# Performance work log

Hardware: AMD Instinct MI355X
Metric: run time of the kernel (lower is better)

Reference implementation:

```python
import jax, jax.numpy as jnp
import numpy as np

N, E = 50000, 800000
DN, DE, H, C = 64, 64, 4, 2
DH = DN // H


def setup_inputs() -> dict:
    key = jax.random.key(0)
    ks = jax.random.split(key, 12)
    def lin(k, fan_in, fan_out):
        return jax.random.normal(k, (fan_in, fan_out), dtype=jnp.float32) / np.sqrt(fan_in)
    return {
        "node_features": jax.random.normal(ks[0], (N, DN), dtype=jnp.float32),
        "edge_features": jax.random.normal(ks[1], (E, DE), dtype=jnp.float32),
        "edge_index": jax.random.randint(ks[2], (2, E), 0, N, dtype=jnp.int64),
        "Wq": lin(ks[3], DN, DN),
        "Wk": lin(ks[4], DN, DN),
        "Wv": lin(ks[5], DN, DN),
        "We": lin(ks[6], DE, DN),
        "Wo": lin(ks[7], DN, DN),
        "W1": lin(ks[8], 2 * DN + DE, DE),
        "b1": jnp.zeros((DE,), dtype=jnp.float32),
        "W2": lin(ks[9], DE, C),
        "b2": jnp.zeros((C,), dtype=jnp.float32),
    }


def reference(node_features, edge_features, edge_index, Wq, Wk, Wv, We, Wo, W1, b1, W2, b2):
    n = node_features.shape[0]
    src, tgt = edge_index[0], edge_index[1]

    # --- NodeAttention: multi-head attention over incoming edges ---
    q = (node_features @ Wq).reshape(n, H, DH)
    k = (node_features @ Wk).reshape(n, H, DH)
    v = (node_features @ Wv).reshape(n, H, DH)
    ep = (edge_features @ We).reshape(-1, H, DH)          # [E,H,DH]

    scores = jnp.sum(q[tgt] * (k[src] + ep), axis=-1) / np.sqrt(DH)  # [E,H]
    smax = jax.ops.segment_max(scores, tgt, num_segments=n)          # [N,H]
    ex = jnp.exp(scores - smax[tgt])
    denom = jax.ops.segment_sum(ex, tgt, num_segments=n)
    alpha = ex / (denom[tgt] + 1e-9)                                 # [E,H]

    msg = (alpha[..., None] * (v[src] + ep)).reshape(-1, H * DH)     # [E,DN]
    agg = jax.ops.segment_sum(msg, tgt, num_segments=n)              # [N,DN]
    new_nodes = node_features + agg @ Wo                             # residual

    # --- edge classifier: gather endpoints, concat edge feats, MLP+GELU ---
    edge_repr = jnp.concatenate([new_nodes[src], new_nodes[tgt], edge_features], axis=-1)
    h = jax.nn.gelu(edge_repr @ W1 + b1, approximate=False)
    return h @ W2 + b2
```

## Files before the change

kernel.cpp:

```cpp
#include <hip/hip_runtime.h>
#include <math.h>

typedef __attribute__((ext_vector_type(8))) short bf16x8;
typedef __attribute__((ext_vector_type(4))) float f32x4;

__device__ __forceinline__ short f2bf(float f) {
    unsigned u = __float_as_uint(f);
    unsigned r = (u + 0x7FFFu + ((u >> 16) & 1u)) >> 16;
    return (short)r;
}

__device__ __forceinline__ int swz(int row, int kbyte) {
    return kbyte ^ ((row & 7) << 4);
}

__global__ __launch_bounds__(256) void qkv_kernel(
    const float* __restrict__ x,
    const float* __restrict__ Wq, const float* __restrict__ Wk, const float* __restrict__ Wv,
    float* __restrict__ q, float* __restrict__ k, float* __restrict__ v, int N)
{
    __shared__ float sW[3][64][64];
    __shared__ float sx[4][64];
    int t = threadIdx.x;
    for (int i = t; i < 4096; i += 256) {
        sW[0][i >> 6][i & 63] = Wq[i];
        sW[1][i >> 6][i & 63] = Wk[i];
        sW[2][i >> 6][i & 63] = Wv[i];
    }
    __syncthreads();
    int c = t & 63, sub = t >> 6;
    for (int base = blockIdx.x * 4; base < N; base += gridDim.x * 4) {
        int n = base + sub;
        if (n < N) sx[sub][c] = x[(size_t)n * 64 + c];
        __syncthreads();
        if (n < N) {
            float aq = 0.f, ak = 0.f, av = 0.f;
            #pragma unroll
            for (int i = 0; i < 64; i++) {
                float xv = sx[sub][i];
                aq += xv * sW[0][i][c];
                ak += xv * sW[1][i][c];
                av += xv * sW[2][i][c];
            }
            q[(size_t)n * 64 + c] = aq;
            k[(size_t)n * 64 + c] = ak;
            v[(size_t)n * 64 + c] = av;
        }
        __syncthreads();
    }
}

__device__ __forceinline__ void stage_w64T(const float* __restrict__ W, short* sWT, int t) {
    for (int i = t; i < 4096; i += 256) {
        int k = i >> 6, n = i & 63;
        short vv = f2bf(W[i]);
        int kb = k * 2;
        int off = n * 128 + (swz(n, kb & ~15) | (kb & 15));
        *(short*)((char*)sWT + off) = vv;
    }
}

__device__ __forceinline__ void ep_mfma(
    const float* __restrict__ ef, const short* sWeT, float* ep_lds,
    size_t tile64, int t)
{
    int lane = t & 63, w = t >> 6;
    f32x4 acc[4];
    #pragma unroll
    for (int nt = 0; nt < 4; nt++) acc[nt] = (f32x4){0.f, 0.f, 0.f, 0.f};

    #pragma unroll
    for (int kk = 0; kk < 2; kk++) {
        const float* base = ef + (tile64 + (size_t)(w * 16 + (lane & 15))) * 64
                               + kk * 32 + (lane >> 4) * 8;
        float4 x0 = *(const float4*)(base);
        float4 x1 = *(const float4*)(base + 4);
        bf16x8 a;
        a[0] = f2bf(x0.x); a[1] = f2bf(x0.y); a[2] = f2bf(x0.z); a[3] = f2bf(x0.w);
        a[4] = f2bf(x1.x); a[5] = f2bf(x1.y); a[6] = f2bf(x1.z); a[7] = f2bf(x1.w);
        #pragma unroll
        for (int nt = 0; nt < 4; nt++) {
            int n = nt * 16 + (lane & 15);
            int kb = kk * 64 + (lane >> 4) * 16;
            bf16x8 b = *(const bf16x8*)((const char*)sWeT + n * 128 + swz(n, kb));
            acc[nt] = __builtin_amdgcn_mfma_f32_16x16x32_bf16(a, b, acc[nt], 0, 0, 0);
        }
    }
    #pragma unroll
    for (int nt = 0; nt < 4; nt++)
        #pragma unroll
        for (int r = 0; r < 4; r++) {
            int row = w * 16 + (lane >> 4) * 4 + r;
            int col = nt * 16 + (lane & 15);
            ep_lds[row * 66 + col] = acc[nt][r];
        }
}

__global__ __launch_bounds__(256) void edge_kernel(
    const float* __restrict__ ef, const int* __restrict__ eidx,
    const float* __restrict__ q, const float* __restrict__ k,
    const float* __restrict__ v, const float* __restrict__ We,
    float* __restrict__ denom, float* __restrict__ agg, int E)
{
    __shared__ short sWeT[4096];
    __shared__ float ep_lds[64 * 66];
    __shared__ float ex_lds[64 * 4];
    __shared__ int sidx[64], tidx[64];
    int t = threadIdx.x;
    stage_w64T(We, sWeT, t);
    __syncthreads();

    int lane = t & 63, w = t >> 6;
    int ntiles = E >> 6;
    for (int tile = blockIdx.x; tile < ntiles; tile += gridDim.x) {
        size_t tile64 = (size_t)tile * 64;
        if (t < 64) {
            sidx[t] = eidx[tile64 + t];
            tidx[t] = eidx[(size_t)E + tile64 + t];
        }
        __syncthreads();
        ep_mfma(ef, sWeT, ep_lds, tile64, t);
        __syncthreads();

        {
            int e_loc = t >> 2, h = t & 3;
            int src = sidx[e_loc], tgt = tidx[e_loc];
            const float4* qp = (const float4*)(q + (size_t)tgt * 64 + h * 16);
            const float4* kp = (const float4*)(k + (size_t)src * 64 + h * 16);
            const float* epp = ep_lds + e_loc * 66 + h * 16;
            float s = 0.f;
            #pragma unroll
            for (int j = 0; j < 4; j++) {
                float4 qq = qp[j];
                float4 kk = kp[j];
                s += qq.x * (kk.x + epp[j * 4 + 0]);
                s += qq.y * (kk.y + epp[j * 4 + 1]);
                s += qq.z * (kk.z + epp[j * 4 + 2]);
                s += qq.w * (kk.w + epp[j * 4 + 3]);
            }
            float ex = __expf(s * 0.25f);
            ex_lds[e_loc * 4 + h] = ex;
            atomicAdd(&denom[(size_t)tgt * 4 + h], ex);
        }
        __syncthreads();

        #pragma unroll 4
        for (int i = 0; i < 16; i++) {
            int e_loc = w * 16 + i;
            int src = sidx[e_loc], tgt = tidx[e_loc];
            float ex = ex_lds[e_loc * 4 + (lane >> 4)];
            float msg = ex * (v[(size_t)src * 64 + lane] + ep_lds[e_loc * 66 + lane]);
            atomicAdd(&agg[(size_t)tgt * 64 + lane], msg);
        }
        __syncthreads();
    }
}

__global__ __launch_bounds__(256) void wo_kernel(
    const float* __restrict__ agg, const float* __restrict__ denom,
    const float* __restrict__ x,
    const float* __restrict__ Wo, float* __restrict__ out, int N)
{
    __shared__ float sW[64][64];
    __shared__ float sx[4][64];
    int t = threadIdx.x;
    for (int i = t; i < 4096; i += 256) sW[i >> 6][i & 63] = Wo[i];
    __syncthreads();
    int c = t & 63, sub = t >> 6;
    for (int base = blockIdx.x * 4; base < N; base += gridDim.x * 4) {
        int n = base + sub;
        if (n < N) {
            float d = denom[(size_t)n * 4 + (c >> 4)] + 1e-9f;
            sx[sub][c] = agg[(size_t)n * 64 + c] / d;
        }
        __syncthreads();
        if (n < N) {
            float acc = 0.f;
            #pragma unroll
            for (int i = 0; i < 64; i++) acc += sx[sub][i] * sW[i][c];
            out[(size_t)n * 64 + c] = x[(size_t)n * 64 + c] + acc;
        }
        __syncthreads();
    }
}

__global__ __launch_bounds__(256, 4) void cls_kernel(
    const float* __restrict__ nn, const float* __restrict__ ef,
    const int* __restrict__ eidx,
    const float* __restrict__ W1, const float* __restrict__ b1,
    const float* __restrict__ W2, const float* __restrict__ b2,
    float* __restrict__ out, int E)
{
    __shared__ short sWt1[64 * 192];
    __shared__ float sW2[128];
    __shared__ float sb1[64];
    __shared__ float sb2[2];
    __shared__ int sidx[64], tidx[64];
    int t = threadIdx.x;
    for (int i = t; i < 192 * 64; i += 256) {
        int k = i >> 6, n = i & 63;
        short vv = f2bf(W1[i]);
        int kb = k * 2;
        int off = n * 384 + (swz(n, kb & ~15) | (kb & 15));
        *(short*)((char*)sWt1 + off) = vv;
    }
    if (t < 128) sW2[t] = W2[t];
    if (t < 64) sb1[t] = b1[t];
    if (t < 2) sb2[t] = b2[t];
    __syncthreads();

    int lane = t & 63, w = t >> 6;
    int ntiles = E >> 6;
    for (int tile = blockIdx.x; tile < ntiles; tile += gridDim.x) {
        size_t tile64 = (size_t)tile * 64;
        if (t < 64) {
            sidx[t] = eidx[tile64 + t];
            tidx[t] = eidx[(size_t)E + tile64 + t];
        }
        __syncthreads();

        f32x4 acc[4];
        #pragma unroll
        for (int nt = 0; nt < 4; nt++) acc[nt] = (f32x4){0.f, 0.f, 0.f, 0.f};

        int e16 = w * 16 + (lane & 15);
        #pragma unroll
        for (int kk = 0; kk < 6; kk++) {
            const float* base;
            if (kk < 2)      base = nn + (size_t)sidx[e16] * 64 + kk * 32;
            else if (kk < 4) base = nn + (size_t)tidx[e16] * 64 + (kk - 2) * 32;
            else             base = ef + (tile64 + (size_t)e16) * 64 + (kk - 4) * 32;
            const float4* p = (const float4*)(base + (lane >> 4) * 8);
            float4 x0 = p[0], x1 = p[1];
            bf16x8 a;
            a[0] = f2bf(x0.x); a[1] = f2bf(x0.y); a[2] = f2bf(x0.z); a[3] = f2bf(x0.w);
            a[4] = f2bf(x1.x); a[5] = f2bf(x1.y); a[6] = f2bf(x1.z); a[7] = f2bf(x1.w);
            #pragma unroll
            for (int nt = 0; nt < 4; nt++) {
                int n = nt * 16 + (lane & 15);
                int kb = kk * 64 + (lane >> 4) * 16;
                bf16x8 b = *(const bf16x8*)((const char*)sWt1 + n * 384 + swz(n, kb));
                acc[nt] = __builtin_amdgcn_mfma_f32_16x16x32_bf16(a, b, acc[nt], 0, 0, 0);
            }
        }

        #pragma unroll
        for (int r = 0; r < 4; r++) {
            float p0 = 0.f, p1 = 0.f;
            #pragma unroll
            for (int nt = 0; nt < 4; nt++) {
                int col = nt * 16 + (lane & 15);
                float h = acc[nt][r] + sb1[col];
                float g = 0.5f * h * (1.f + erff(h * 0.70710678118654752f));
                p0 += g * sW2[col * 2 + 0];
                p1 += g * sW2[col * 2 + 1];
            }
            #pragma unroll
            for (int o = 1; o < 16; o <<= 1) {
                p0 += __shfl_xor(p0, o, 64);
                p1 += __shfl_xor(p1, o, 64);
            }
            if ((lane & 15) == 0) {
                int row = w * 16 + (lane >> 4) * 4 + r;
                out[(tile64 + (size_t)row) * 2 + 0] = p0 + sb2[0];
                out[(tile64 + (size_t)row) * 2 + 1] = p1 + sb2[1];
            }
        }
        __syncthreads();
    }
}

extern "C" void kernel_launch(void* const* d_in, const int* in_sizes, int n_in,
                              void* d_out, int out_size, void* d_ws, size_t ws_size,
                              hipStream_t stream)
{
    const float* node = (const float*)d_in[0];
    const float* ef   = (const float*)d_in[1];
    const int*   eidx = (const int*)d_in[2];
    const float* Wq   = (const float*)d_in[3];
    const float* Wk   = (const float*)d_in[4];
    const float* Wv   = (const float*)d_in[5];
    const float* We   = (const float*)d_in[6];
    const float* Wo   = (const float*)d_in[7];
    const float* W1   = (const float*)d_in[8];
    const float* b1   = (const float*)d_in[9];
    const float* W2   = (const float*)d_in[10];
    const float* b2   = (const float*)d_in[11];
    float* out = (float*)d_out;

    int N = in_sizes[0] / 64;
    int E = in_sizes[1] / 64;
    size_t N64 = (size_t)N * 64;

    float* q     = (float*)d_ws;
    float* k     = q + N64;
    float* v     = k + N64;
    float* newn  = v + N64;
    float* agg   = newn + N64;
    float* denom = agg + N64;

    hipMemsetAsync(agg, 0, (N64 + (size_t)N * 4) * sizeof(float), stream);

    qkv_kernel<<<512, 256, 0, stream>>>(node, Wq, Wk, Wv, q, k, v, N);
    edge_kernel<<<2048, 256, 0, stream>>>(ef, eidx, q, k, v, We, denom, agg, E);
    wo_kernel<<<512, 256, 0, stream>>>(agg, denom, node, Wo, newn, N);
    cls_kernel<<<2048, 256, 0, stream>>>(newn, ef, eidx, W1, b1, W2, b2, out, E);
}
```

Before: 674.0 us.

## Sort edges by target and pre-reduce per-wave attention scatter; store new nodes in bf16

Adds a counting sort of edges by target node (histogram, single-block scan, atomic scatter) so the edge kernel processes target-grouped edges. Each wave then accumulates runs of edges sharing a target in registers and issues one atomic per run instead of one per edge, for both agg and denom. The updated node features are also written as bf16, so the classifier gathers half the bytes and skips the conversion. The cost is three extra launches, including a serial one-block scan over 50k nodes, and random-order gathers of edge features in the edge kernel.

New measurement: 693.0 us. 1.03x slower.

```diff
diff --git a/kernel.cpp b/kernel.cpp
--- a/kernel.cpp
+++ b/kernel.cpp
@@ -12,6 +12,49 @@
 
 __device__ __forceinline__ int swz(int row, int kbyte) {
     return kbyte ^ ((row & 7) << 4);
+}
+
+__global__ __launch_bounds__(256) void hist_kernel(
+    const int* __restrict__ eidx, int* __restrict__ cnt, int E)
+{
+    for (long e = (long)blockIdx.x * blockDim.x + threadIdx.x; e < E;
+         e += (long)gridDim.x * blockDim.x)
+        atomicAdd(&cnt[eidx[E + e]], 1);
+}
+
+__global__ __launch_bounds__(1024) void scan_kernel(
+    const int* __restrict__ cnt, int* __restrict__ cursor, int N)
+{
+    __shared__ int pa[1024], pb[1024];
+    int t = threadIdx.x;
+    int chunk = (N + 1023) >> 10;
+    int lo = t * chunk, hi = min(lo + chunk, N);
+    int s = 0;
+    for (int j = lo; j < hi; j++) s += cnt[j];
+    pa[t] = s;
+    __syncthreads();
+    int* src = pa; int* dst = pb;
+    for (int off = 1; off < 1024; off <<= 1) {
+        int val = src[t];
+        if (t >= off) val += src[t - off];
+        dst[t] = val;
+        __syncthreads();
+        int* tmp = src; src = dst; dst = tmp;
+    }
+    int excl = (t == 0) ? 0 : src[t - 1];
+    for (int j = lo; j < hi; j++) { cursor[j] = excl; excl += cnt[j]; }
+}
+
+__global__ __launch_bounds__(256) void scatter_kernel(
+    const int* __restrict__ eidx, int* __restrict__ cursor,
+    int* __restrict__ sorted, int E)
+{
+    for (long e = (long)blockIdx.x * blockDim.x + threadIdx.x; e < E;
+         e += (long)gridDim.x * blockDim.x) {
+        int tg = eidx[E + e];
+        int pos = atomicAdd(&cursor[tg], 1);
+        sorted[pos] = (int)e;
+    }
 }
 
 __global__ __launch_bounds__(256) void qkv_kernel(
@@ -60,44 +103,9 @@
     }
 }
 
-__device__ __forceinline__ void ep_mfma(
-    const float* __restrict__ ef, const short* sWeT, float* ep_lds,
-    size_t tile64, int t)
-{
-    int lane = t & 63, w = t >> 6;
-    f32x4 acc[4];
-    #pragma unroll
-    for (int nt = 0; nt < 4; nt++) acc[nt] = (f32x4){0.f, 0.f, 0.f, 0.f};
-
-    #pragma unroll
-    for (int kk = 0; kk < 2; kk++) {
-        const float* base = ef + (tile64 + (size_t)(w * 16 + (lane & 15))) * 64
-                               + kk * 32 + (lane >> 4) * 8;
-        float4 x0 = *(const float4*)(base);
-        float4 x1 = *(const float4*)(base + 4);
-        bf16x8 a;
-        a[0] = f2bf(x0.x); a[1] = f2bf(x0.y); a[2] = f2bf(x0.z); a[3] = f2bf(x0.w);
-        a[4] = f2bf(x1.x); a[5] = f2bf(x1.y); a[6] = f2bf(x1.z); a[7] = f2bf(x1.w);
-        #pragma unroll
-        for (int nt = 0; nt < 4; nt++) {
-            int n = nt * 16 + (lane & 15);
-            int kb = kk * 64 + (lane >> 4) * 16;
-            bf16x8 b = *(const bf16x8*)((const char*)sWeT + n * 128 + swz(n, kb));
-            acc[nt] = __builtin_amdgcn_mfma_f32_16x16x32_bf16(a, b, acc[nt], 0, 0, 0);
-        }
-    }
-    #pragma unroll
-    for (int nt = 0; nt < 4; nt++)
-        #pragma unroll
-        for (int r = 0; r < 4; r++) {
-            int row = w * 16 + (lane >> 4) * 4 + r;
-            int col = nt * 16 + (lane & 15);
-            ep_lds[row * 66 + col] = acc[nt][r];
-        }
-}
-
 __global__ __launch_bounds__(256) void edge_kernel(
     const float* __restrict__ ef, const int* __restrict__ eidx,
+    const int* __restrict__ sorted,
     const float* __restrict__ q, const float* __restrict__ k,
     const float* __restrict__ v, const float* __restrict__ We,
     float* __restrict__ denom, float* __restrict__ agg, int E)
@@ -105,9 +113,154 @@
     __shared__ short sWeT[4096];
     __shared__ float ep_lds[64 * 66];
     __shared__ float ex_lds[64 * 4];
+    __shared__ int sedge[64], sidx[64], tidx[64];
+    int t = threadIdx.x;
+    stage_w64T(We, sWeT, t);
+    __syncthreads();
+
+    int lane = t & 63, w = t >> 6;
+    int ntiles = E >> 6;
+    for (int tile = blockIdx.x; tile < ntiles; tile += gridDim.x) {
+        size_t tile64 = (size_t)tile * 64;
+        if (t < 64) {
+            int se = sorted[tile64 + t];
+            sedge[t] = se;
+            sidx[t] = eidx[se];
+            tidx[t] = eidx[E + se];
+        }
+        __syncthreads();
+
+        {
+            f32x4 acc[4];
+            #pragma unroll
+            for (int nt = 0; nt < 4; nt++) acc[nt] = (f32x4){0.f, 0.f, 0.f, 0.f};
+            int erow = sedge[w * 16 + (lane & 15)];
+            #pragma unroll
+            for (int kk = 0; kk < 2; kk++) {
+                const float* base = ef + (size_t)erow * 64 + kk * 32 + (lane >> 4) * 8;
+                float4 x0 = *(const float4*)(base);
+                float4 x1 = *(const float4*)(base + 4);
+                bf16x8 a;
+                a[0] = f2bf(x0.x); a[1] = f2bf(x0.y); a[2] = f2bf(x0.z); a[3] = f2bf(x0.w);
+                a[4] = f2bf(x1.x); a[5] = f2bf(x1.y); a[6] = f2bf(x1.z); a[7] = f2bf(x1.w);
+                #pragma unroll
+                for (int nt = 0; nt < 4; nt++) {
+                    int n = nt * 16 + (lane & 15);
+                    int kb = kk * 64 + (lane >> 4) * 16;
+                    bf16x8 b = *(const bf16x8*)((const char*)sWeT + n * 128 + swz(n, kb));
+                    acc[nt] = __builtin_amdgcn_mfma_f32_16x16x32_bf16(a, b, acc[nt], 0, 0, 0);
+                }
+            }
+            #pragma unroll
+            for (int nt = 0; nt < 4; nt++)
+                #pragma unroll
+                for (int r = 0; r < 4; r++) {
+                    int row = w * 16 + (lane >> 4) * 4 + r;
+                    int col = nt * 16 + (lane & 15);
+                    ep_lds[row * 66 + col] = acc[nt][r];
+                }
+        }
+        __syncthreads();
+
+        {
+            int e_loc = t >> 2, h = t & 3;
+            int src = sidx[e_loc], tgt = tidx[e_loc];
+            const float4* qp = (const float4*)(q + (size_t)tgt * 64 + h * 16);
+            const float4* kp = (const float4*)(k + (size_t)src * 64 + h * 16);
+            const float* epp = ep_lds + e_loc * 66 + h * 16;
+            float s = 0.f;
+            #pragma unroll
+            for (int j = 0; j < 4; j++) {
+                float4 qq = qp[j];
+                float4 kk = kp[j];
+                s += qq.x * (kk.x + epp[j * 4 + 0]);
+                s += qq.y * (kk.y + epp[j * 4 + 1]);
+                s += qq.z * (kk.z + epp[j * 4 + 2]);
+                s += qq.w * (kk.w + epp[j * 4 + 3]);
+            }
+            ex_lds[e_loc * 4 + h] = __expf(s * 0.25f);
+        }
+        __syncthreads();
+
+        {
+            int h = lane >> 4;
+            float vv[16];
+            #pragma unroll
+            for (int i = 0; i < 16; i++)
+                vv[i] = v[(size_t)sidx[w * 16 + i] * 64 + lane];
+            int cur = tidx[w * 16];
+            float acc = 0.f, den = 0.f;
+            #pragma unroll
+            for (int i = 0; i < 16; i++) {
+                int e_loc = w * 16 + i;
+                int tg = tidx[e_loc];
+                if (tg != cur) {
+                    atomicAdd(&agg[(size_t)cur * 64 + lane], acc);
+                    if ((lane & 15) == 0) atomicAdd(&denom[(size_t)cur * 4 + h], den);
+                    acc = 0.f; den = 0.f; cur = tg;
+                }
+                float ex = ex_lds[e_loc * 4 + h];
+                acc += ex * (vv[i] + ep_lds[e_loc * 66 + lane]);
+                den += ex;
+            }
+            atomicAdd(&agg[(size_t)cur * 64 + lane], acc);
+            if ((lane & 15) == 0) atomicAdd(&denom[(size_t)cur * 4 + h], den);
+        }
+        __syncthreads();
+    }
+}
+
+__global__ __launch_bounds__(256) void wo_kernel(
+    const float* __restrict__ agg, const float* __restrict__ denom,
+    const float* __restrict__ x,
+    const float* __restrict__ Wo, short* __restrict__ out_bf, int N)
+{
+    __shared__ float sW[64][64];
+    __shared__ float sx[4][64];
+    int t = threadIdx.x;
+    for (int i = t; i < 4096; i += 256) sW[i >> 6][i & 63] = Wo[i];
+    __syncthreads();
+    int c = t & 63, sub = t >> 6;
+    for (int base = blockIdx.x * 4; base < N; base += gridDim.x * 4) {
+        int n = base + sub;
+        if (n < N) {
+            float d = denom[(size_t)n * 4 + (c >> 4)] + 1e-9f;
+            sx[sub][c] = agg[(size_t)n * 64 + c] / d;
+        }
+        __syncthreads();
+        if (n < N) {
+            float acc = 0.f;
+            #pragma unroll
+            for (int i = 0; i < 64; i++) acc += sx[sub][i] * sW[i][c];
+            out_bf[(size_t)n * 64 + c] = f2bf(x[(size_t)n * 64 + c] + acc);
+        }
+        __syncthreads();
+    }
+}
+
+__global__ __launch_bounds__(256, 4) void cls_kernel(
+    const short* __restrict__ nnb, const float* __restrict__ ef,
+    const int* __restrict__ eidx,
+    const float* __restrict__ W1, const float* __restrict__ b1,
+    const float* __restrict__ W2, const float* __restrict__ b2,
+    float* __restrict__ out, int E)
+{
+    __shared__ short sWt1[64 * 192];
+    __shared__ float sW2[128];
+    __shared__ float sb1[64];
+    __shared__ float sb2[2];
     __shared__ int sidx[64], tidx[64];
     int t = threadIdx.x;
-    stage_w64T(We, sWeT, t);
+    for (int i = t; i < 192 * 64; i += 256) {
+        int k = i >> 6, n = i & 63;
+        short vv = f2bf(W1[i]);
+        int kb = k * 2;
+        int off = n * 384 + (swz(n, kb & ~15) | (kb & 15));
+        *(short*)((char*)sWt1 + off) = vv;
+    }
+    if (t < 128) sW2[t] = W2[t];
+    if (t < 64) sb1[t] = b1[t];
+    if (t < 2) sb2[t] = b2[t];
     __syncthreads();
 
     int lane = t & 63, w = t >> 6;
@@ -119,105 +272,6 @@
             tidx[t] = eidx[(size_t)E + tile64 + t];
         }
         __syncthreads();
-        ep_mfma(ef, sWeT, ep_lds, tile64, t);
-        __syncthreads();
-
-        {
-            int e_loc = t >> 2, h = t & 3;
-            int src = sidx[e_loc], tgt = tidx[e_loc];
-            const float4* qp = (const float4*)(q + (size_t)tgt * 64 + h * 16);
-            const float4* kp = (const float4*)(k + (size_t)src * 64 + h * 16);
-            const float* epp = ep_lds + e_loc * 66 + h * 16;
-            float s = 0.f;
-            #pragma unroll
-            for (int j = 0; j < 4; j++) {
-                float4 qq = qp[j];
-                float4 kk = kp[j];
-                s += qq.x * (kk.x + epp[j * 4 + 0]);
-                s += qq.y * (kk.y + epp[j * 4 + 1]);
-                s += qq.z * (kk.z + epp[j * 4 + 2]);
-                s += qq.w * (kk.w + epp[j * 4 + 3]);
-            }
-            float ex = __expf(s * 0.25f);
-            ex_lds[e_loc * 4 + h] = ex;
-            atomicAdd(&denom[(size_t)tgt * 4 + h], ex);
-        }
-        __syncthreads();
-
-        #pragma unroll 4
-        for (int i = 0; i < 16; i++) {
-            int e_loc = w * 16 + i;
-            int src = sidx[e_loc], tgt = tidx[e_loc];
-            float ex = ex_lds[e_loc * 4 + (lane >> 4)];
-            float msg = ex * (v[(size_t)src * 64 + lane] + ep_lds[e_loc * 66 + lane]);
-            atomicAdd(&agg[(size_t)tgt * 64 + lane], msg);
-        }
-        __syncthreads();
-    }
-}
-
-__global__ __launch_bounds__(256) void wo_kernel(
-    const float* __restrict__ agg, const float* __restrict__ denom,
-    const float* __restrict__ x,
-    const float* __restrict__ Wo, float* __restrict__ out, int N)
-{
-    __shared__ float sW[64][64];
-    __shared__ float sx[4][64];
-    int t = threadIdx.x;
-    for (int i = t; i < 4096; i += 256) sW[i >> 6][i & 63] = Wo[i];
-    __syncthreads();
-    int c = t & 63, sub = t >> 6;
-    for (int base = blockIdx.x * 4; base < N; base += gridDim.x * 4) {
-        int n = base + sub;
-        if (n < N) {
-            float d = denom[(size_t)n * 4 + (c >> 4)] + 1e-9f;
-            sx[sub][c] = agg[(size_t)n * 64 + c] / d;
-        }
-        __syncthreads();
-        if (n < N) {
-            float acc = 0.f;
-            #pragma unroll
-            for (int i = 0; i < 64; i++) acc += sx[sub][i] * sW[i][c];
-            out[(size_t)n * 64 + c] = x[(size_t)n * 64 + c] + acc;
-        }
-        __syncthreads();
-    }
-}
-
-__global__ __launch_bounds__(256, 4) void cls_kernel(
-    const float* __restrict__ nn, const float* __restrict__ ef,
-    const int* __restrict__ eidx,
-    const float* __restrict__ W1, const float* __restrict__ b1,
-    const float* __restrict__ W2, const float* __restrict__ b2,
-    float* __restrict__ out, int E)
-{
-    __shared__ short sWt1[64 * 192];
-    __shared__ float sW2[128];
-    __shared__ float sb1[64];
-    __shared__ float sb2[2];
-    __shared__ int sidx[64], tidx[64];
-    int t = threadIdx.x;
-    for (int i = t; i < 192 * 64; i += 256) {
-        int k = i >> 6, n = i & 63;
-        short vv = f2bf(W1[i]);
-        int kb = k * 2;
-        int off = n * 384 + (swz(n, kb & ~15) | (kb & 15));
-        *(short*)((char*)sWt1 + off) = vv;
-    }
-    if (t < 128) sW2[t] = W2[t];
-    if (t < 64) sb1[t] = b1[t];
-    if (t < 2) sb2[t] = b2[t];
-    __syncthreads();
-
-    int lane = t & 63, w = t >> 6;
-    int ntiles = E >> 6;
-    for (int tile = blockIdx.x; tile < ntiles; tile += gridDim.x) {
-        size_t tile64 = (size_t)tile * 64;
-        if (t < 64) {
-            sidx[t] = eidx[tile64 + t];
-            tidx[t] = eidx[(size_t)E + tile64 + t];
-        }
-        __syncthreads();
 
         f32x4 acc[4];
         #pragma unroll
@@ -226,15 +280,17 @@
         int e16 = w * 16 + (lane & 15);
         #pragma unroll
         for (int kk = 0; kk < 6; kk++) {
-            const float* base;
-            if (kk < 2)      base = nn + (size_t)sidx[e16] * 64 + kk * 32;
-            else if (kk < 4) base = nn + (size_t)tidx[e16] * 64 + (kk - 2) * 32;
-            else             base = ef + (tile64 + (size_t)e16) * 64 + (kk - 4) * 32;
-            const float4* p = (const float4*)(base + (lane >> 4) * 8);
-            float4 x0 = p[0], x1 = p[1];
             bf16x8 a;
-            a[0] = f2bf(x0.x); a[1] = f2bf(x0.y); a[2] = f2bf(x0.z); a[3] = f2bf(x0.w);
-            a[4] = f2bf(x1.x); a[5] = f2bf(x1.y); a[6] = f2bf(x1.z); a[7] = f2bf(x1.w);
+            if (kk < 4) {
+                int nd = (kk < 2) ? sidx[e16] : tidx[e16];
+                a = *(const bf16x8*)(nnb + (size_t)nd * 64 + (kk & 1) * 32 + (lane >> 4) * 8);
+            } else {
+                const float* base = ef + (tile64 + (size_t)e16) * 64 + (kk - 4) * 32;
+                const float4* p = (const float4*)(base + (lane >> 4) * 8);
+                float4 x0 = p[0], x1 = p[1];
+                a[0] = f2bf(x0.x); a[1] = f2bf(x0.y); a[2] = f2bf(x0.z); a[3] = f2bf(x0.w);
+                a[4] = f2bf(x1.x); a[5] = f2bf(x1.y); a[6] = f2bf(x1.z); a[7] = f2bf(x1.w);
+            }
             #pragma unroll
             for (int nt = 0; nt < 4; nt++) {
                 int n = nt * 16 + (lane & 15);
@@ -292,17 +348,23 @@
     int E = in_sizes[1] / 64;
     size_t N64 = (size_t)N * 64;
 
-    float* q     = (float*)d_ws;
-    float* k     = q + N64;
-    float* v     = k + N64;
-    float* newn  = v + N64;
-    float* agg   = newn + N64;
-    float* denom = agg + N64;
-
-    hipMemsetAsync(agg, 0, (N64 + (size_t)N * 4) * sizeof(float), stream);
-
+    float* q      = (float*)d_ws;
+    float* k      = q + N64;
+    float* v      = k + N64;
+    float* agg    = v + N64;
+    float* denom  = agg + N64;
+    int*   cnt    = (int*)(denom + (size_t)N * 4);
+    int*   cursor = cnt + N;
+    int*   sorted = cursor + N;
+    short* newnb  = (short*)(sorted + E);
+
+    hipMemsetAsync(agg, 0, (N64 + (size_t)N * 4 + (size_t)N) * 4, stream);
+
+    hist_kernel<<<2048, 256, 0, stream>>>(eidx, cnt, E);
+    scan_kernel<<<1, 1024, 0, stream>>>(cnt, cursor, N);
+    scatter_kernel<<<2048, 256, 0, stream>>>(eidx, cursor, sorted, E);
     qkv_kernel<<<512, 256, 0, stream>>>(node, Wq, Wk, Wv, q, k, v, N);
-    edge_kernel<<<2048, 256, 0, stream>>>(ef, eidx, q, k, v, We, denom, agg, E);
-    wo_kernel<<<512, 256, 0, stream>>>(agg, denom, node, Wo, newn, N);
-    cls_kernel<<<2048, 256, 0, stream>>>(newn, ef, eidx, W1, b1, W2, b2, out, E);
-}
+    edge_kernel<<<2048, 256, 0, stream>>>(ef, eidx, sorted, q, k, v, We, denom, agg, E);
+    wo_kernel<<<512, 256, 0, stream>>>(agg, denom, node, Wo, newnb, N);
+    cls_kernel<<<2048, 256, 0, stream>>>(newnb, ef, eidx, W1, b1, W2, b2, out, E);
+}
```
